# Optimization experiments

Measured on AMD Instinct MI355X. Metric: run time of the kernel, lower is better.

Reference implementation:

```python
import jax, jax.numpy as jnp
import numpy as np

D_MODEL = 1024
N_HEADS = 16
CAUSAL = True
NEG_INF = -1e10


def get_freqs(seq_len, n_dim):
    # standard RoPE frequencies: theta_i = 10000^(-2i/n_dim), angles[s, i] = s * theta_i
    inv_freq = 1.0 / (10000.0 ** (jnp.arange(0, n_dim, 2, dtype=jnp.float32) / n_dim))
    t = jnp.arange(seq_len, dtype=jnp.float32)
    return jnp.outer(t, inv_freq)  # [S, n_dim//2]


def rope(x, freqs):
    # x: [B, S, H, n_dim]; interleaved pair rotation
    B, S, H, Dh = x.shape
    xr = x.reshape(B, S, H, Dh // 2, 2)
    x1, x2 = xr[..., 0], xr[..., 1]
    cos = jnp.cos(freqs)[None, :, None, :]  # [1,S,1,Dh/2]
    sin = jnp.sin(freqs)[None, :, None, :]
    o1 = x1 * cos - x2 * sin
    o2 = x1 * sin + x2 * cos
    return jnp.stack([o1, o2], axis=-1).reshape(B, S, H, Dh)


def setup_inputs() -> dict:
    key = jax.random.key(0)
    ks = jax.random.split(key, 5)
    B, S, D = 2, 2048, D_MODEL
    return {
        "x": jax.random.normal(ks[0], (B, S, D), dtype=jnp.float32),
        "qw": jax.random.normal(ks[1], (D, D), dtype=jnp.float32),
        "kw": jax.random.normal(ks[2], (D, D), dtype=jnp.float32),
        "vw": jax.random.normal(ks[3], (D, D), dtype=jnp.float32),
        "ow": jax.random.normal(ks[4], (D, D), dtype=jnp.float32),
    }


def reference(x, qw, kw, vw, ow):
    B, S, D = x.shape
    H = N_HEADS
    Dh = D // H
    Q = (x @ qw).reshape(B, S, H, Dh)
    K = (x @ kw).reshape(B, S, H, Dh)
    V = (x @ vw).reshape(B, S, H, Dh)
    freqs = get_freqs(S, Dh)
    Q = rope(Q, freqs)
    K = rope(K, freqs)
    # [B,H,S,S] scores, scaled by sqrt(d_model) as in the original (not sqrt(head_dim))
    scores = jnp.einsum("bqhd,bkhd->bhqk", Q, K) / jnp.sqrt(jnp.float32(D))
    scores = scores.astype(jnp.float32)
    if CAUSAL:
        causal = jnp.tril(jnp.ones((S, S), dtype=bool))
        scores = jnp.where(causal[None, None, :, :], scores, NEG_INF)
    weights = jax.nn.softmax(scores, axis=-1)
    attn = jnp.einsum("bhqk,bkhd->bqhd", weights, V).reshape(B, S, D)
    return attn @ ow
```

## Files before the change

### kernel.cpp

```cpp
#include <hip/hip_runtime.h>
#include <hip/hip_bf16.h>
#include <math.h>

#define SEQ    2048
#define BATCH  2
#define DM     1024
#define NH     16
#define DH     64
#define BS_ROWS 4096
#define KDIM   1024

typedef __attribute__((ext_vector_type(8))) short short8v;
typedef __attribute__((ext_vector_type(4))) float f32x4;
typedef unsigned short ushort_t;

__device__ __forceinline__ unsigned short f2bf(float f) {
  union { float f; unsigned u; } v; v.f = f;
  unsigned r = (v.u + 0x7FFF + ((v.u >> 16) & 1)) >> 16;
  return (unsigned short)r;
}
__device__ __forceinline__ float bf2f(unsigned short h) {
  union { unsigned u; float f; } v; v.u = ((unsigned)h) << 16;
  return v.f;
}

__device__ __forceinline__ void gl16(const void* g, void* l) {
  __builtin_amdgcn_global_load_lds(
      (const __attribute__((address_space(1))) unsigned int*)g,
      (__attribute__((address_space(3))) unsigned int*)l,
      16, 0, 0);
}

__global__ __launch_bounds__(256)
void split_f32(const float* __restrict__ src, ushort_t* __restrict__ h,
               ushort_t* __restrict__ l, int n8)
{
  const int i = blockIdx.x * 256 + threadIdx.x;
  if (i >= n8) return;
  const float4 v0 = ((const float4*)src)[2 * i];
  const float4 v1 = ((const float4*)src)[2 * i + 1];
  const float vals[8] = {v0.x, v0.y, v0.z, v0.w, v1.x, v1.y, v1.z, v1.w};
  short8v hv, lv;
  #pragma unroll
  for (int e = 0; e < 8; e++) {
    const unsigned short hb = f2bf(vals[e]);
    hv[e] = (short)hb;
    lv[e] = (short)f2bf(vals[e] - bf2f(hb));
  }
  ((short8v*)h)[i] = hv;
  ((short8v*)l)[i] = lv;
}

__global__ __launch_bounds__(256)
void wtrans(const float* __restrict__ w0, const float* __restrict__ w1,
            const float* __restrict__ w2, const float* __restrict__ w3,
            ushort_t* __restrict__ WT)
{
  __shared__ float tile[64][65];
  const int z = blockIdx.z;
  const float* __restrict__ W = (z == 0) ? w0 : (z == 1) ? w1 : (z == 2) ? w2 : w3;
  ushort_t* __restrict__ Oh = WT + (size_t)z * 2097152;
  ushort_t* __restrict__ Ol = Oh + 1048576;

  const int n0 = blockIdx.x * 64, k0 = blockIdx.y * 64;
  const int r  = threadIdx.x >> 2;
  const int c0 = (threadIdx.x & 3) * 16;

  #pragma unroll
  for (int i = 0; i < 4; i++) {
    const float4 v = *(const float4*)&W[(size_t)(k0 + r) * KDIM + n0 + c0 + 4 * i];
    tile[r][c0 + 4 * i + 0] = v.x; tile[r][c0 + 4 * i + 1] = v.y;
    tile[r][c0 + 4 * i + 2] = v.z; tile[r][c0 + 4 * i + 3] = v.w;
  }
  __syncthreads();

  #pragma unroll
  for (int c = 0; c < 2; c++) {
    short8v hv, lv;
    #pragma unroll
    for (int e = 0; e < 8; e++) {
      const float x = tile[c0 + c * 8 + e][r];
      const unsigned short hb = f2bf(x);
      hv[e] = (short)hb;
      lv[e] = (short)f2bf(x - bf2f(hb));
    }
    const size_t off = (size_t)(n0 + r) * KDIM + k0 + c0 + c * 8;
    *(short8v*)&Oh[off] = hv;
    if (z <= 2) *(short8v*)&Ol[off] = lv;
  }
}

#define MF(a_, b_, c_) __builtin_amdgcn_mfma_f32_16x16x32_bf16(a_, b_, c_, 0, 0, 0)

#define M16(p_, q_)                                                          \
  c00=MF(p_##0,q_##0,c00); c01=MF(p_##0,q_##1,c01); c02=MF(p_##0,q_##2,c02); c03=MF(p_##0,q_##3,c03); \
  c10=MF(p_##1,q_##0,c10); c11=MF(p_##1,q_##1,c11); c12=MF(p_##1,q_##2,c12); c13=MF(p_##1,q_##3,c13); \
  c20=MF(p_##2,q_##0,c20); c21=MF(p_##2,q_##1,c21); c22=MF(p_##2,q_##2,c22); c23=MF(p_##2,q_##3,c23); \
  c30=MF(p_##3,q_##0,c30); c31=MF(p_##3,q_##1,c31); c32=MF(p_##3,q_##2,c32); c33=MF(p_##3,q_##3,c33);

__global__ __launch_bounds__(256, 2)
void gemm_qkv(const ushort_t* __restrict__ Ahp, const ushort_t* __restrict__ Alp,
              const ushort_t* __restrict__ WT,
              ushort_t* __restrict__ Qh, ushort_t* __restrict__ Ql,
              ushort_t* __restrict__ Kh, ushort_t* __restrict__ Kl,
              ushort_t* __restrict__ Vt)
{
  const int mode = blockIdx.z;
  const bool qk = (mode <= 1);
  const ushort_t* __restrict__ Bhp = WT + (size_t)mode * 2097152;
  const ushort_t* __restrict__ Blp = Bhp + 1048576;

  __shared__ ushort_t A2[128][64];
  __shared__ ushort_t B2[128][64];

  const int t = threadIdx.x;
  const int lane = t & 63, w = t >> 6;
  const int l4 = lane & 15, lh = lane >> 4;
  const int wm = w >> 1, wn = w & 1;
  const int row0 = blockIdx.y * 128, col0 = blockIdx.x * 128;

  const int srow = t >> 3;
  const int spc  = t & 7;
  const int slc  = spc ^ (srow & 7);
  const int koff = (slc & 3) * 8;
  const ushort_t* __restrict__ sA = (slc < 4) ? Ahp : Alp;
  const ushort_t* __restrict__ sB = (slc < 4) ? Bhp : (qk ? Blp : Bhp);

  const int pcA = lh ^ (l4 & 7);

  f32x4 c00 = {0,0,0,0}, c01 = {0,0,0,0}, c02 = {0,0,0,0}, c03 = {0,0,0,0};
  f32x4 c10 = {0,0,0,0}, c11 = {0,0,0,0}, c12 = {0,0,0,0}, c13 = {0,0,0,0};
  f32x4 c20 = {0,0,0,0}, c21 = {0,0,0,0}, c22 = {0,0,0,0}, c23 = {0,0,0,0};
  f32x4 c30 = {0,0,0,0}, c31 = {0,0,0,0}, c32 = {0,0,0,0}, c33 = {0,0,0,0};

  const int rA = wm * 64 + l4;
  const int rB = wn * 64 + l4;

  for (int k0 = 0; k0 < KDIM; k0 += 32) {
    #pragma unroll
    for (int i = 0; i < 4; i++) {
      gl16(sA + (size_t)(row0 + i * 32 + srow) * KDIM + k0 + koff,
           (char*)A2 + i * 4096 + w * 1024);
      gl16(sB + (size_t)(col0 + i * 32 + srow) * KDIM + k0 + koff,
           (char*)B2 + i * 4096 + w * 1024);
    }
    __syncthreads();

    const short8v ah0 = *(const short8v*)&A2[rA +  0][pcA * 8];
    const short8v ah1 = *(const short8v*)&A2[rA + 16][pcA * 8];
    const short8v ah2 = *(const short8v*)&A2[rA + 32][pcA * 8];
    const short8v ah3 = *(const short8v*)&A2[rA + 48][pcA * 8];
    const short8v al0 = *(const short8v*)&A2[rA +  0][(pcA ^ 4) * 8];
    const short8v al1 = *(const short8v*)&A2[rA + 16][(pcA ^ 4) * 8];
    const short8v al2 = *(const short8v*)&A2[rA + 32][(pcA ^ 4) * 8];
    const short8v al3 = *(const short8v*)&A2[rA + 48][(pcA ^ 4) * 8];
    const short8v bh0 = *(const short8v*)&B2[rB +  0][pcA * 8];
    const short8v bh1 = *(const short8v*)&B2[rB + 16][pcA * 8];
    const short8v bh2 = *(const short8v*)&B2[rB + 32][pcA * 8];
    const short8v bh3 = *(const short8v*)&B2[rB + 48][pcA * 8];

    M16(ah, bh)
    if (qk) {
      const short8v bl0 = *(const short8v*)&B2[rB +  0][(pcA ^ 4) * 8];
      const short8v bl1 = *(const short8v*)&B2[rB + 16][(pcA ^ 4) * 8];
      const short8v bl2 = *(const short8v*)&B2[rB + 32][(pcA ^ 4) * 8];
      const short8v bl3 = *(const short8v*)&B2[rB + 48][(pcA ^ 4) * 8];
      M16(ah, bl)
    }
    M16(al, bh)
    __syncthreads();
  }

  f32x4 acc[4][4];
  acc[0][0]=c00; acc[0][1]=c01; acc[0][2]=c02; acc[0][3]=c03;
  acc[1][0]=c10; acc[1][1]=c11; acc[1][2]=c12; acc[1][3]=c13;
  acc[2][0]=c20; acc[2][1]=c21; acc[2][2]=c22; acc[2][3]=c23;
  acc[3][0]=c30; acc[3][1]=c31; acc[3][2]=c32; acc[3][3]=c33;

  if (mode <= 1) {
    const float scale = (mode == 0) ? 0.03125f : 1.0f;
    ushort_t* __restrict__ Hp = (mode == 0) ? Qh : Kh;
    ushort_t* __restrict__ Lp = (mode == 0) ? Ql : Kl;
    #pragma unroll
    for (int mf = 0; mf < 4; mf++)
      #pragma unroll
      for (int nf = 0; nf < 4; nf++) {
        const int col = col0 + wn * 64 + nf * 16 + l4;
        const int p = (col & (DH - 1)) >> 1;
        const float fr = exp2f((float)p * -0.41524101186092030f);
        const float sgn = (col & 1) ? 1.0f : -1.0f;
        #pragma unroll
        for (int j = 0; j < 4; j++) {
          const int grow = row0 + wm * 64 + mf * 16 + lh * 4 + j;
          const float s = (float)(grow & (SEQ - 1));
          float sn, cs;
          sincosf(s * fr, &sn, &cs);
          const float val = acc[mf][nf][j];
          const float par = __shfl_xor(val, 1);
          const float out = val * cs + par * (sgn * sn);
          const float xsc = out * scale;
          const unsigned short hb = f2bf(xsc);
          Hp[(size_t)grow * DM + col] = hb;
          Lp[(size_t)grow * DM + col] = f2bf(xsc - bf2f(hb));
        }
      }
  } else {
    #pragma unroll
    for (int mf = 0; mf < 4; mf++)
      #pragma unroll
      for (int nf = 0; nf < 4; nf++) {
        const int col = col0 + wn * 64 + nf * 16 + l4;
        const int hh = col >> 6, dd = col & (DH - 1);
        #pragma unroll
        for (int j = 0; j < 4; j++) {
          const int grow = row0 + wm * 64 + mf * 16 + lh * 4 + j;
          const int b = grow >> 11, ss = grow & (SEQ - 1);
          Vt[((size_t)((b * NH + hh) * DH + dd)) * SEQ + ss] = f2bf(acc[mf][nf][j]);
        }
      }
  }
}

__global__ __launch_bounds__(256, 2)
void gemm_out(const ushort_t* __restrict__ Ahp, const ushort_t* __restrict__ WT,
              float* __restrict__ Cf)
{
  const ushort_t* __restrict__ Bhp = WT + (size_t)3 * 2097152;

  __shared__ ushort_t A3[128][32];
  __shared__ ushort_t B3[64][32];

  const int t = threadIdx.x;
  const int lane = t & 63, w = t >> 6;
  const int l4 = lane & 15, lh = lane >> 4;
  const int wm = w >> 1, wn = w & 1;
  const int row0 = blockIdx.y * 128, col0 = blockIdx.x * 64;

  const int srow = t >> 2;
  const int spc  = t & 3;
  const int slc  = spc ^ (srow & 3);
  const int koff = slc * 8;

  const int pc4 = lh ^ (l4 & 3);

  f32x4 c00={0,0,0,0}, c01={0,0,0,0};
  f32x4 c10={0,0,0,0}, c11={0,0,0,0};
  f32x4 c20={0,0,0,0}, c21={0,0,0,0};
  f32x4 c30={0,0,0,0}, c31={0,0,0,0};

  const int rA = wm * 64 + l4;
  const int rB = wn * 32 + l4;

  for (int k0 = 0; k0 < KDIM; k0 += 32) {
    #pragma unroll
    for (int i = 0; i < 2; i++)
      gl16(Ahp + (size_t)(row0 + i * 64 + srow) * KDIM + k0 + koff,
           (char*)A3 + i * 4096 + w * 1024);
    gl16(Bhp + (size_t)(col0 + srow) * KDIM + k0 + koff,
         (char*)B3 + w * 1024);
    __syncthreads();

    const short8v ah0 = *(const short8v*)&A3[rA +  0][pc4 * 8];
    const short8v ah1 = *(const short8v*)&A3[rA + 16][pc4 * 8];
    const short8v ah2 = *(const short8v*)&A3[rA + 32][pc4 * 8];
    const short8v ah3 = *(const short8v*)&A3[rA + 48][pc4 * 8];
    const short8v bh0 = *(const short8v*)&B3[rB +  0][pc4 * 8];
    const short8v bh1 = *(const short8v*)&B3[rB + 16][pc4 * 8];

    c00 = MF(ah0, bh0, c00); c01 = MF(ah0, bh1, c01);
    c10 = MF(ah1, bh0, c10); c11 = MF(ah1, bh1, c11);
    c20 = MF(ah2, bh0, c20); c21 = MF(ah2, bh1, c21);
    c30 = MF(ah3, bh0, c30); c31 = MF(ah3, bh1, c31);
    __syncthreads();
  }

  f32x4 acc[4][2];
  acc[0][0]=c00; acc[0][1]=c01; acc[1][0]=c10; acc[1][1]=c11;
  acc[2][0]=c20; acc[2][1]=c21; acc[3][0]=c30; acc[3][1]=c31;

  #pragma unroll
  for (int mf = 0; mf < 4; mf++)
    #pragma unroll
    for (int nf = 0; nf < 2; nf++) {
      const int col = col0 + wn * 32 + nf * 16 + l4;
      #pragma unroll
      for (int j = 0; j < 4; j++) {
        const int grow = row0 + wm * 64 + mf * 16 + lh * 4 + j;
        Cf[(size_t)grow * DM + col] = acc[mf][nf][j];
      }
    }
}

__global__ __launch_bounds__(256, 4)
void attn_mfma(const ushort_t* __restrict__ Qh, const ushort_t* __restrict__ Ql,
               const ushort_t* __restrict__ Kh, const ushort_t* __restrict__ Kl,
               const ushort_t* __restrict__ Vt, ushort_t* __restrict__ AAh)
{
  __shared__ __align__(16) ushort_t Khl[2][2][64][32];
  __shared__ __align__(16) ushort_t Vtl[64][72];
  __shared__ __align__(16) ushort_t Pl[4][16][72];

  const int t = threadIdx.x;
  const int lane = t & 63, wv = t >> 6;
  const int l4 = lane & 15, lh = lane >> 4;
  const int qblk = blockIdx.x, bh = blockIdx.y;
  const int bI = bh >> 4, h = bh & 15;
  const int q0w = qblk * 64 + wv * 16;
  const int qrow = q0w + l4;

  const int kr = t >> 2, kc = t & 3;
  const int ckw = (kc ^ ((kr >> 1) & 3)) * 8;
  const int csr = (lh ^ ((l4 >> 1) & 3)) * 8;

  short8v aqh0, aqh1, aql0, aql1;
  {
    const size_t qoff = (size_t)((bI * SEQ) + qrow) * DM + h * DH;
    aqh0 = *(const short8v*)&Qh[qoff + lh * 8];
    aqh1 = *(const short8v*)&Qh[qoff + 32 + lh * 8];
    aql0 = *(const short8v*)&Ql[qoff + lh * 8];
    aql1 = *(const short8v*)&Ql[qoff + 32 + lh * 8];
  }

  f32x4 o0 = {0,0,0,0}, o1 = {0,0,0,0}, o2 = {0,0,0,0}, o3 = {0,0,0,0};
  float mrun = -1e30f, lsum = 0.f;

  const ushort_t* __restrict__ Vg = Vt + (size_t)bh * DH * SEQ;
  const size_t kgbase = (size_t)(bI * SEQ + kr) * DM + h * DH + kc * 8;
  const int nt = qblk + 1;

  short8v rkh0, rkh1, rkl0, rkl1, rv0, rv1;

#define LOADR(kt_) {                                                         \
    const size_t ko = kgbase + (size_t)(kt_) * 64 * DM;                      \
    rkh0 = *(const short8v*)&Kh[ko];                                         \
    rkh1 = *(const short8v*)&Kh[ko + 32];                                    \
    rkl0 = *(const short8v*)&Kl[ko];                                         \
    rkl1 = *(const short8v*)&Kl[ko + 32];                                    \
    const size_t vo = (size_t)kr * SEQ + (kt_) * 64 + kc * 8;                \
    rv0 = *(const short8v*)&Vg[vo];                                          \
    rv1 = *(const short8v*)&Vg[vo + 32]; }

#define WRITES() {                                                           \
    *(short8v*)&Khl[0][0][kr][ckw] = rkh0;                                   \
    *(short8v*)&Khl[0][1][kr][ckw] = rkh1;                                   \
    *(short8v*)&Khl[1][0][kr][ckw] = rkl0;                                   \
    *(short8v*)&Khl[1][1][kr][ckw] = rkl1;                                   \
    *(short8v*)&Vtl[kr][kc * 8]      = rv0;                                  \
    *(short8v*)&Vtl[kr][kc * 8 + 32] = rv1; }

#define QKSTEP(sN, n) {                                                      \
    const short8v kh0 = *(const short8v*)&Khl[0][0][(n)*16 + l4][csr];       \
    const short8v kh1 = *(const short8v*)&Khl[0][1][(n)*16 + l4][csr];       \
    const short8v kl0 = *(const short8v*)&Khl[1][0][(n)*16 + l4][csr];       \
    const short8v kl1 = *(const short8v*)&Khl[1][1][(n)*16 + l4][csr];       \
    sN = MF(kh0, aqh0, sN);                                                  \
    sN = MF(kh0, aql0, sN);                                                  \
    sN = MF(kl0, aqh0, sN);                                                  \
    sN = MF(kh1, aqh1, sN);                                                  \
    sN = MF(kh1, aql1, sN);                                                  \
    sN = MF(kl1, aqh1, sN); }

#define MASKN(sN, n) {                                                       \
    const int kb0 = kb + (n)*16 + lh*4;                                      \
    if (kb0 + 0 > qrow) sN[0] = -1e30f;                                      \
    if (kb0 + 1 > qrow) sN[1] = -1e30f;                                      \
    if (kb0 + 2 > qrow) sN[2] = -1e30f;                                      \
    if (kb0 + 3 > qrow) sN[3] = -1e30f; }

#define EXPN(sN) {                                                           \
    sN[0] = __expf(sN[0] - nm); sN[1] = __expf(sN[1] - nm);                  \
    sN[2] = __expf(sN[2] - nm); sN[3] = __expf(sN[3] - nm); }

#define PWRITE(sN, n) {                                                      \
    unsigned pa, pb;                                                         \
    asm("v_cvt_pk_bf16_f32 %0, %1, %2" : "=v"(pa) : "v"(sN[0]), "v"(sN[1]));\
    asm("v_cvt_pk_bf16_f32 %0, %1, %2" : "=v"(pb) : "v"(sN[2]), "v"(sN[3]));\
    *(unsigned*)&Pl[wv][l4][(n)*16 + lh*4]     = pa;                         \
    *(unsigned*)&Pl[wv][l4][(n)*16 + lh*4 + 2] = pb; }

#define PVSTEP(kb2) {                                                        \
    const short8v ap  = *(const short8v*)&Pl[wv][l4][(kb2)*32 + lh*8];       \
    const short8v bv0 = *(const short8v*)&Vtl[ 0 + l4][(kb2)*32 + lh*8];     \
    const short8v bv1 = *(const short8v*)&Vtl[16 + l4][(kb2)*32 + lh*8];     \
    const short8v bv2 = *(const short8v*)&Vtl[32 + l4][(kb2)*32 + lh*8];     \
    const short8v bv3 = *(const short8v*)&Vtl[48 + l4][(kb2)*32 + lh*8];     \
    o0 = MF(bv0, ap, o0);                                                    \
    o1 = MF(bv1, ap, o1);                                                    \
    o2 = MF(bv2, ap, o2);                                                    \
    o3 = MF(bv3, ap, o3); }

  LOADR(0); WRITES();
  __syncthreads();

  for (int kt = 0; kt < nt; kt++) {
    const bool pf = (kt + 1 < nt);
    if (pf) LOADR(kt + 1);

    f32x4 s0 = {0,0,0,0}, s1 = {0,0,0,0}, s2 = {0,0,0,0}, s3 = {0,0,0,0};
    QKSTEP(s0, 0) QKSTEP(s1, 1) QKSTEP(s2, 2) QKSTEP(s3, 3)

    const int kb = kt * 64;
    MASKN(s0, 0) MASKN(s1, 1) MASKN(s2, 2) MASKN(s3, 3)

    float vmax = fmaxf(fmaxf(fmaxf(s0[0], s0[1]), fmaxf(s0[2], s0[3])),
                       fmaxf(fmaxf(s1[0], s1[1]), fmaxf(s1[2], s1[3])));
    vmax = fmaxf(vmax, fmaxf(fmaxf(s2[0], s2[1]), fmaxf(s2[2], s2[3])));
    vmax = fmaxf(vmax, fmaxf(fmaxf(s3[0], s3[1]), fmaxf(s3[2], s3[3])));
    vmax = fmaxf(vmax, __shfl_xor(vmax, 16));
    vmax = fmaxf(vmax, __shfl_xor(vmax, 32));

    const float nm = fmaxf(mrun, vmax);
    const float corr = __expf(mrun - nm);
    mrun = nm;

    EXPN(s0) EXPN(s1) EXPN(s2) EXPN(s3)

    float rs = (s0[0] + s0[1]) + (s0[2] + s0[3]) + (s1[0] + s1[1]) + (s1[2] + s1[3])
             + (s2[0] + s2[1]) + (s2[2] + s2[3]) + (s3[0] + s3[1]) + (s3[2] + s3[3]);
    rs += __shfl_xor(rs, 16);
    rs += __shfl_xor(rs, 32);
    lsum = lsum * corr + rs;

    o0 *= corr; o1 *= corr; o2 *= corr; o3 *= corr;

    PWRITE(s0, 0) PWRITE(s1, 1) PWRITE(s2, 2) PWRITE(s3, 3)

    PVSTEP(0) PVSTEP(1)

    if (pf) {
      __syncthreads();
      WRITES();
      __syncthreads();
    }
  }

  const float inv = 1.0f / lsum;
  const size_t rowoff = ((size_t)(bI * SEQ + qrow)) * DM + h * DH;
  #pragma unroll
  for (int df = 0; df < 4; df++) {
    const f32x4 ov = (df == 0) ? o0 : (df == 1) ? o1 : (df == 2) ? o2 : o3;
    #pragma unroll
    for (int jp = 0; jp < 2; jp++) {
      const float x0 = ov[2 * jp] * inv;
      const float x1 = ov[2 * jp + 1] * inv;
      const unsigned short h0 = f2bf(x0), h1 = f2bf(x1);
      const size_t col = rowoff + df * 16 + lh * 4 + 2 * jp;
      *(unsigned*)&AAh[col] = (unsigned)h0 | ((unsigned)h1 << 16);
    }
  }
#undef LOADR
#undef WRITES
#undef QKSTEP
#undef MASKN
#undef EXPN
#undef PWRITE
#undef PVSTEP
}

extern "C" void kernel_launch(void* const* d_in, const int* in_sizes, int n_in,
                              void* d_out, int out_size, void* d_ws, size_t ws_size,
                              hipStream_t stream) {
  const float* x  = (const float*)d_in[0];
  const float* qw = (const float*)d_in[1];
  const float* kw = (const float*)d_in[2];
  const float* vw = (const float*)d_in[3];
  const float* ow = (const float*)d_in[4];

  char* ws = (char*)d_ws;
  ushort_t* Xh  = (ushort_t*)ws;
  ushort_t* Xl  = Xh + 4194304;
  ushort_t* AAh = Xh;
  ushort_t* Kh  = (ushort_t*)(ws + (16u << 20));
  ushort_t* Kl  = Kh + 4194304;
  ushort_t* Vt  = (ushort_t*)(ws + (32u << 20));
  ushort_t* WT  = (ushort_t*)(ws + (40u << 20));
  ushort_t* Qh  = (ushort_t*)d_out;
  ushort_t* Ql  = Qh + 4194304;
  float*    out = (float*)d_out;

  split_f32<<<dim3(2048), dim3(256), 0, stream>>>(x, Xh, Xl, 524288);
  wtrans<<<dim3(16, 16, 4), dim3(256), 0, stream>>>(qw, kw, vw, ow, WT);
  gemm_qkv<<<dim3(8, 32, 3), dim3(256), 0, stream>>>(
      Xh, Xl, WT, Qh, Ql, Kh, Kl, Vt);
  attn_mfma<<<dim3(SEQ / 64, BATCH * NH), dim3(256), 0, stream>>>(
      Qh, Ql, Kh, Kl, Vt, AAh);
  gemm_out<<<dim3(16, 32), dim3(256), 0, stream>>>(AAh, WT, out);
}
```

Baseline: 213.6 us.

## Enlarge QKV GEMM tile to 256x256 with double-buffered LDS prefetch

The QKV projection GEMM moves from 128x128 tiles with 256 threads to 256x256 tiles with 512 threads (8 waves, each owning 128x64 outputs). It double-buffers the LDS tiles so the next K-slice's global-to-LDS loads are issued while MFMAs on the current slice run, and it raises wave priority around the MFMA bursts. The goal is better operand reuse and hiding of global load latency. The cost is 128 KB of LDS per block, which allows only one block per CU, and a grid of 192 blocks, fewer than the number of CUs, so some CUs sit idle. Register pressure also rises.

```diff
diff --git a/kernel.cpp b/kernel.cpp
--- a/kernel.cpp
+++ b/kernel.cpp
@@ -92,13 +92,7 @@
 
 #define MF(a_, b_, c_) __builtin_amdgcn_mfma_f32_16x16x32_bf16(a_, b_, c_, 0, 0, 0)
 
-#define M16(p_, q_)                                                          \
-  c00=MF(p_##0,q_##0,c00); c01=MF(p_##0,q_##1,c01); c02=MF(p_##0,q_##2,c02); c03=MF(p_##0,q_##3,c03); \
-  c10=MF(p_##1,q_##0,c10); c11=MF(p_##1,q_##1,c11); c12=MF(p_##1,q_##2,c12); c13=MF(p_##1,q_##3,c13); \
-  c20=MF(p_##2,q_##0,c20); c21=MF(p_##2,q_##1,c21); c22=MF(p_##2,q_##2,c22); c23=MF(p_##2,q_##3,c23); \
-  c30=MF(p_##3,q_##0,c30); c31=MF(p_##3,q_##1,c31); c32=MF(p_##3,q_##2,c32); c33=MF(p_##3,q_##3,c33);
-
-__global__ __launch_bounds__(256, 2)
+__global__ __launch_bounds__(512, 2)
 void gemm_qkv(const ushort_t* __restrict__ Ahp, const ushort_t* __restrict__ Alp,
               const ushort_t* __restrict__ WT,
               ushort_t* __restrict__ Qh, ushort_t* __restrict__ Ql,
@@ -110,92 +104,128 @@
   const ushort_t* __restrict__ Bhp = WT + (size_t)mode * 2097152;
   const ushort_t* __restrict__ Blp = Bhp + 1048576;
 
-  __shared__ ushort_t A2[128][64];
-  __shared__ ushort_t B2[128][64];
+  __shared__ ushort_t A2[2][256][64];
+  __shared__ ushort_t B2[2][256][64];
 
   const int t = threadIdx.x;
-  const int lane = t & 63, w = t >> 6;
-  const int l4 = lane & 15, lh = lane >> 4;
-  const int wm = w >> 1, wn = w & 1;
-  const int row0 = blockIdx.y * 128, col0 = blockIdx.x * 128;
+  const int l = t & 63, w = t >> 6;
+  const int l4 = l & 15, lh = l >> 4;
+  const int wm = w >> 2, wn = w & 3;
+  const int row0 = blockIdx.y * 256, col0 = blockIdx.x * 256;
 
   const int srow = t >> 3;
   const int spc  = t & 7;
   const int slc  = spc ^ (srow & 7);
   const int koff = (slc & 3) * 8;
   const ushort_t* __restrict__ sA = (slc < 4) ? Ahp : Alp;
-  const ushort_t* __restrict__ sB = (slc < 4) ? Bhp : (qk ? Blp : Bhp);
+  const ushort_t* __restrict__ sB = (slc < 4) ? Bhp : Blp;
 
   const int pcA = lh ^ (l4 & 7);
 
-  f32x4 c00 = {0,0,0,0}, c01 = {0,0,0,0}, c02 = {0,0,0,0}, c03 = {0,0,0,0};
-  f32x4 c10 = {0,0,0,0}, c11 = {0,0,0,0}, c12 = {0,0,0,0}, c13 = {0,0,0,0};
-  f32x4 c20 = {0,0,0,0}, c21 = {0,0,0,0}, c22 = {0,0,0,0}, c23 = {0,0,0,0};
-  f32x4 c30 = {0,0,0,0}, c31 = {0,0,0,0}, c32 = {0,0,0,0}, c33 = {0,0,0,0};
-
-  const int rA = wm * 64 + l4;
-  const int rB = wn * 64 + l4;
-
-  for (int k0 = 0; k0 < KDIM; k0 += 32) {
-    #pragma unroll
-    for (int i = 0; i < 4; i++) {
-      gl16(sA + (size_t)(row0 + i * 32 + srow) * KDIM + k0 + koff,
-           (char*)A2 + i * 4096 + w * 1024);
-      gl16(sB + (size_t)(col0 + i * 32 + srow) * KDIM + k0 + koff,
-           (char*)B2 + i * 4096 + w * 1024);
-    }
-    __syncthreads();
-
-    const short8v ah0 = *(const short8v*)&A2[rA +  0][pcA * 8];
-    const short8v ah1 = *(const short8v*)&A2[rA + 16][pcA * 8];
-    const short8v ah2 = *(const short8v*)&A2[rA + 32][pcA * 8];
-    const short8v ah3 = *(const short8v*)&A2[rA + 48][pcA * 8];
-    const short8v al0 = *(const short8v*)&A2[rA +  0][(pcA ^ 4) * 8];
-    const short8v al1 = *(const short8v*)&A2[rA + 16][(pcA ^ 4) * 8];
-    const short8v al2 = *(const short8v*)&A2[rA + 32][(pcA ^ 4) * 8];
-    const short8v al3 = *(const short8v*)&A2[rA + 48][(pcA ^ 4) * 8];
-    const short8v bh0 = *(const short8v*)&B2[rB +  0][pcA * 8];
-    const short8v bh1 = *(const short8v*)&B2[rB + 16][pcA * 8];
-    const short8v bh2 = *(const short8v*)&B2[rB + 32][pcA * 8];
-    const short8v bh3 = *(const short8v*)&B2[rB + 48][pcA * 8];
-
-    M16(ah, bh)
-    if (qk) {
-      const short8v bl0 = *(const short8v*)&B2[rB +  0][(pcA ^ 4) * 8];
-      const short8v bl1 = *(const short8v*)&B2[rB + 16][(pcA ^ 4) * 8];
-      const short8v bl2 = *(const short8v*)&B2[rB + 32][(pcA ^ 4) * 8];
-      const short8v bl3 = *(const short8v*)&B2[rB + 48][(pcA ^ 4) * 8];
-      M16(ah, bl)
-    }
-    M16(al, bh)
-    __syncthreads();
-  }
-
-  f32x4 acc[4][4];
+  f32x4 c00={0,0,0,0},c01={0,0,0,0},c02={0,0,0,0},c03={0,0,0,0},
+        c04={0,0,0,0},c05={0,0,0,0},c06={0,0,0,0},c07={0,0,0,0};
+  f32x4 c10={0,0,0,0},c11={0,0,0,0},c12={0,0,0,0},c13={0,0,0,0},
+        c14={0,0,0,0},c15={0,0,0,0},c16={0,0,0,0},c17={0,0,0,0};
+  f32x4 c20={0,0,0,0},c21={0,0,0,0},c22={0,0,0,0},c23={0,0,0,0},
+        c24={0,0,0,0},c25={0,0,0,0},c26={0,0,0,0},c27={0,0,0,0};
+  f32x4 c30={0,0,0,0},c31={0,0,0,0},c32={0,0,0,0},c33={0,0,0,0},
+        c34={0,0,0,0},c35={0,0,0,0},c36={0,0,0,0},c37={0,0,0,0};
+
+#define STAGE_A(buf_, k0_) { _Pragma("unroll")                               \
+    for (int i = 0; i < 4; i++)                                              \
+      gl16(sA + (size_t)(row0 + i * 64 + srow) * KDIM + (k0_) + koff,        \
+           (char*)A2[buf_] + i * 8192 + w * 1024); }
+#define STAGE_B(buf_, k0_) { _Pragma("unroll")                               \
+    for (int i = 0; i < 4; i++)                                              \
+      gl16(sB + (size_t)(col0 + i * 64 + srow) * KDIM + (k0_) + koff,        \
+           (char*)B2[buf_] + i * 8192 + w * 1024); }
+
+#define M4N(a_, B_, mf_)                                                     \
+  c0##mf_ = MF(a_, B_##0, c0##mf_); c1##mf_ = MF(a_, B_##1, c1##mf_);        \
+  c2##mf_ = MF(a_, B_##2, c2##mf_); c3##mf_ = MF(a_, B_##3, c3##mf_);
+
+#define APHASE(mfA_, mfB_) {                                                 \
+    const int raA = wm * 128 + mfA_ * 16 + l4;                               \
+    const int raB = wm * 128 + mfB_ * 16 + l4;                               \
+    const short8v ahA = *(const short8v*)&A2[cur][raA][pcA * 8];             \
+    const short8v alA = *(const short8v*)&A2[cur][raA][(pcA ^ 4) * 8];       \
+    const short8v ahB = *(const short8v*)&A2[cur][raB][pcA * 8];             \
+    const short8v alB = *(const short8v*)&A2[cur][raB][(pcA ^ 4) * 8];       \
+    __builtin_amdgcn_s_setprio(1);                                           \
+    M4N(ahA, bh, mfA_)                                                       \
+    if (qk) { M4N(ahA, bl, mfA_) }                                           \
+    M4N(alA, bh, mfA_)                                                       \
+    M4N(ahB, bh, mfB_)                                                       \
+    if (qk) { M4N(ahB, bl, mfB_) }                                           \
+    M4N(alB, bh, mfB_)                                                       \
+    __builtin_amdgcn_s_setprio(0);                                           \
+    __builtin_amdgcn_s_barrier(); }
+
+  STAGE_A(0, 0);
+  STAGE_B(0, 0);
+
+  for (int kt = 0; kt < 32; kt++) {
+    const int cur = kt & 1;
+    const int nxt = cur ^ 1;
+    const int k0n = (kt + 1) * 32;
+
+    asm volatile("s_waitcnt vmcnt(0)" ::: "memory");
+    __builtin_amdgcn_s_barrier();
+
+    const int rB0 = wn * 64 +  0 + l4;
+    const int rB1 = wn * 64 + 16 + l4;
+    const int rB2 = wn * 64 + 32 + l4;
+    const int rB3 = wn * 64 + 48 + l4;
+    const short8v bh0 = *(const short8v*)&B2[cur][rB0][pcA * 8];
+    const short8v bh1 = *(const short8v*)&B2[cur][rB1][pcA * 8];
+    const short8v bh2 = *(const short8v*)&B2[cur][rB2][pcA * 8];
+    const short8v bh3 = *(const short8v*)&B2[cur][rB3][pcA * 8];
+    const short8v bl0 = *(const short8v*)&B2[cur][rB0][(pcA ^ 4) * 8];
+    const short8v bl1 = *(const short8v*)&B2[cur][rB1][(pcA ^ 4) * 8];
+    const short8v bl2 = *(const short8v*)&B2[cur][rB2][(pcA ^ 4) * 8];
+    const short8v bl3 = *(const short8v*)&B2[cur][rB3][(pcA ^ 4) * 8];
+
+    if (kt < 31) STAGE_A(nxt, k0n);
+    APHASE(0, 1)
+    if (kt < 31) STAGE_B(nxt, k0n);
+    APHASE(2, 3)
+    APHASE(4, 5)
+    APHASE(6, 7)
+  }
+#undef STAGE_A
+#undef STAGE_B
+#undef M4N
+#undef APHASE
+
+  f32x4 acc[4][8];
   acc[0][0]=c00; acc[0][1]=c01; acc[0][2]=c02; acc[0][3]=c03;
+  acc[0][4]=c04; acc[0][5]=c05; acc[0][6]=c06; acc[0][7]=c07;
   acc[1][0]=c10; acc[1][1]=c11; acc[1][2]=c12; acc[1][3]=c13;
+  acc[1][4]=c14; acc[1][5]=c15; acc[1][6]=c16; acc[1][7]=c17;
   acc[2][0]=c20; acc[2][1]=c21; acc[2][2]=c22; acc[2][3]=c23;
+  acc[2][4]=c24; acc[2][5]=c25; acc[2][6]=c26; acc[2][7]=c27;
   acc[3][0]=c30; acc[3][1]=c31; acc[3][2]=c32; acc[3][3]=c33;
+  acc[3][4]=c34; acc[3][5]=c35; acc[3][6]=c36; acc[3][7]=c37;
 
   if (mode <= 1) {
     const float scale = (mode == 0) ? 0.03125f : 1.0f;
     ushort_t* __restrict__ Hp = (mode == 0) ? Qh : Kh;
     ushort_t* __restrict__ Lp = (mode == 0) ? Ql : Kl;
     #pragma unroll
-    for (int mf = 0; mf < 4; mf++)
+    for (int nf = 0; nf < 4; nf++) {
+      const int col = col0 + wn * 64 + nf * 16 + l4;
+      const int p = (col & (DH - 1)) >> 1;
+      const float fr = exp2f((float)p * -0.41524101186092030f);
+      const float sgn = (col & 1) ? 1.0f : -1.0f;
       #pragma unroll
-      for (int nf = 0; nf < 4; nf++) {
-        const int col = col0 + wn * 64 + nf * 16 + l4;
-        const int p = (col & (DH - 1)) >> 1;
-        const float fr = exp2f((float)p * -0.41524101186092030f);
-        const float sgn = (col & 1) ? 1.0f : -1.0f;
+      for (int mf = 0; mf < 8; mf++) {
         #pragma unroll
         for (int j = 0; j < 4; j++) {
-          const int grow = row0 + wm * 64 + mf * 16 + lh * 4 + j;
+          const int grow = row0 + wm * 128 + mf * 16 + lh * 4 + j;
           const float s = (float)(grow & (SEQ - 1));
           float sn, cs;
           sincosf(s * fr, &sn, &cs);
-          const float val = acc[mf][nf][j];
+          const float val = acc[nf][mf][j];
           const float par = __shfl_xor(val, 1);
           const float out = val * cs + par * (sgn * sn);
           const float xsc = out * scale;
@@ -204,20 +234,22 @@
           Lp[(size_t)grow * DM + col] = f2bf(xsc - bf2f(hb));
         }
       }
+    }
   } else {
     #pragma unroll
-    for (int mf = 0; mf < 4; mf++)
+    for (int nf = 0; nf < 4; nf++) {
+      const int col = col0 + wn * 64 + nf * 16 + l4;
+      const int hh = col >> 6, dd = col & (DH - 1);
       #pragma unroll
-      for (int nf = 0; nf < 4; nf++) {
-        const int col = col0 + wn * 64 + nf * 16 + l4;
-        const int hh = col >> 6, dd = col & (DH - 1);
+      for (int mf = 0; mf < 8; mf++) {
         #pragma unroll
         for (int j = 0; j < 4; j++) {
-          const int grow = row0 + wm * 64 + mf * 16 + lh * 4 + j;
+          const int grow = row0 + wm * 128 + mf * 16 + lh * 4 + j;
           const int b = grow >> 11, ss = grow & (SEQ - 1);
-          Vt[((size_t)((b * NH + hh) * DH + dd)) * SEQ + ss] = f2bf(acc[mf][nf][j]);
+          Vt[((size_t)((b * NH + hh) * DH + dd)) * SEQ + ss] = f2bf(acc[nf][mf][j]);
         }
       }
+    }
   }
 }
 
@@ -480,7 +512,7 @@
 
   split_f32<<<dim3(2048), dim3(256), 0, stream>>>(x, Xh, Xl, 524288);
   wtrans<<<dim3(16, 16, 4), dim3(256), 0, stream>>>(qw, kw, vw, ow, WT);
-  gemm_qkv<<<dim3(8, 32, 3), dim3(256), 0, stream>>>(
+  gemm_qkv<<<dim3(4, 16, 3), dim3(512), 0, stream>>>(
       Xh, Xl, WT, Qh, Ql, Kh, Kl, Vt);
   attn_mfma<<<dim3(SEQ / 64, BATCH * NH), dim3(256), 0, stream>>>(
       Qh, Ql, Kh, Kl, Vt, AAh);
```

Result: slower. 237.2 us (+11.0%).

## Double-buffer LDS tiles in QKV GEMM to overlap global loads with MFMA

Applied to the files above, without the earlier changes.

The QKV projection GEMM now uses two LDS buffers for the A and B tiles. It issues the direct-to-LDS loads for the next K-slice before computing on the current one, waiting on vmcnt(8) and a bare s_barrier instead of a full __syncthreads. This is meant to hide global-load latency behind MFMA work. LDS use doubles to 64KB per block, which may reduce occupancy under launch_bounds(256,2). Correctness depends on the manual waitcnt accounting and on the LDS-DMA ordering holding.

```diff
diff --git a/kernel.cpp b/kernel.cpp
--- a/kernel.cpp
+++ b/kernel.cpp
@@ -110,8 +110,8 @@
   const ushort_t* __restrict__ Bhp = WT + (size_t)mode * 2097152;
   const ushort_t* __restrict__ Blp = Bhp + 1048576;
 
-  __shared__ ushort_t A2[128][64];
-  __shared__ ushort_t B2[128][64];
+  __shared__ ushort_t A2[2][128][64];
+  __shared__ ushort_t B2[2][128][64];
 
   const int t = threadIdx.x;
   const int lane = t & 63, w = t >> 6;
@@ -136,40 +136,52 @@
   const int rA = wm * 64 + l4;
   const int rB = wn * 64 + l4;
 
-  for (int k0 = 0; k0 < KDIM; k0 += 32) {
-    #pragma unroll
-    for (int i = 0; i < 4; i++) {
-      gl16(sA + (size_t)(row0 + i * 32 + srow) * KDIM + k0 + koff,
-           (char*)A2 + i * 4096 + w * 1024);
-      gl16(sB + (size_t)(col0 + i * 32 + srow) * KDIM + k0 + koff,
-           (char*)B2 + i * 4096 + w * 1024);
+#define STAGE(buf_, k0_) { _Pragma("unroll")                                 \
+    for (int i = 0; i < 4; i++) {                                            \
+      gl16(sA + (size_t)(row0 + i * 32 + srow) * KDIM + (k0_) + koff,        \
+           (char*)A2[buf_] + i * 4096 + w * 1024);                           \
+      gl16(sB + (size_t)(col0 + i * 32 + srow) * KDIM + (k0_) + koff,        \
+           (char*)B2[buf_] + i * 4096 + w * 1024);                           \
+    } }
+
+  STAGE(0, 0);
+
+  for (int kt = 0; kt < 32; kt++) {
+    const int cur = kt & 1;
+    if (kt < 31) {
+      STAGE(cur ^ 1, (kt + 1) * 32);
+      asm volatile("s_waitcnt vmcnt(8)" ::: "memory");
+    } else {
+      asm volatile("s_waitcnt vmcnt(0)" ::: "memory");
     }
-    __syncthreads();
-
-    const short8v ah0 = *(const short8v*)&A2[rA +  0][pcA * 8];
-    const short8v ah1 = *(const short8v*)&A2[rA + 16][pcA * 8];
-    const short8v ah2 = *(const short8v*)&A2[rA + 32][pcA * 8];
-    const short8v ah3 = *(const short8v*)&A2[rA + 48][pcA * 8];
-    const short8v al0 = *(const short8v*)&A2[rA +  0][(pcA ^ 4) * 8];
-    const short8v al1 = *(const short8v*)&A2[rA + 16][(pcA ^ 4) * 8];
-    const short8v al2 = *(const short8v*)&A2[rA + 32][(pcA ^ 4) * 8];
-    const short8v al3 = *(const short8v*)&A2[rA + 48][(pcA ^ 4) * 8];
-    const short8v bh0 = *(const short8v*)&B2[rB +  0][pcA * 8];
-    const short8v bh1 = *(const short8v*)&B2[rB + 16][pcA * 8];
-    const short8v bh2 = *(const short8v*)&B2[rB + 32][pcA * 8];
-    const short8v bh3 = *(const short8v*)&B2[rB + 48][pcA * 8];
+    __builtin_amdgcn_s_barrier();
+
+    const short8v ah0 = *(const short8v*)&A2[cur][rA +  0][pcA * 8];
+    const short8v ah1 = *(const short8v*)&A2[cur][rA + 16][pcA * 8];
+    const short8v ah2 = *(const short8v*)&A2[cur][rA + 32][pcA * 8];
+    const short8v ah3 = *(const short8v*)&A2[cur][rA + 48][pcA * 8];
+    const short8v al0 = *(const short8v*)&A2[cur][rA +  0][(pcA ^ 4) * 8];
+    const short8v al1 = *(const short8v*)&A2[cur][rA + 16][(pcA ^ 4) * 8];
+    const short8v al2 = *(const short8v*)&A2[cur][rA + 32][(pcA ^ 4) * 8];
+    const short8v al3 = *(const short8v*)&A2[cur][rA + 48][(pcA ^ 4) * 8];
+    const short8v bh0 = *(const short8v*)&B2[cur][rB +  0][pcA * 8];
+    const short8v bh1 = *(const short8v*)&B2[cur][rB + 16][pcA * 8];
+    const short8v bh2 = *(const short8v*)&B2[cur][rB + 32][pcA * 8];
+    const short8v bh3 = *(const short8v*)&B2[cur][rB + 48][pcA * 8];
 
     M16(ah, bh)
     if (qk) {
-      const short8v bl0 = *(const short8v*)&B2[rB +  0][(pcA ^ 4) * 8];
-      const short8v bl1 = *(const short8v*)&B2[rB + 16][(pcA ^ 4) * 8];
-      const short8v bl2 = *(const short8v*)&B2[rB + 32][(pcA ^ 4) * 8];
-      const short8v bl3 = *(const short8v*)&B2[rB + 48][(pcA ^ 4) * 8];
+      const short8v bl0 = *(const short8v*)&B2[cur][rB +  0][(pcA ^ 4) * 8];
+      const short8v bl1 = *(const short8v*)&B2[cur][rB + 16][(pcA ^ 4) * 8];
+      const short8v bl2 = *(const short8v*)&B2[cur][rB + 32][(pcA ^ 4) * 8];
+      const short8v bl3 = *(const short8v*)&B2[cur][rB + 48][(pcA ^ 4) * 8];
       M16(ah, bl)
     }
     M16(al, bh)
-    __syncthreads();
-  }
+
+    __builtin_amdgcn_s_barrier();
+  }
+#undef STAGE
 
   f32x4 acc[4][4];
   acc[0][0]=c00; acc[0][1]=c01; acc[0][2]=c02; acc[0][3]=c03;
```

New measurement: 224.2 us. 5.0% more time.
